# Kernel tuning notes

Hardware: AMD Instinct MI355X
Metric: run time of the kernel (lower is better)

Reference implementation:

```python
import jax, jax.numpy as jnp
import numpy as np
import math

WINDOW = 1024
B, H, E, D = 4, 8, 64, 64


def setup_inputs() -> dict:
    key = jax.random.key(0)
    kq, kk, kv, ks = jax.random.split(key, 4)
    queries = jax.random.normal(kq, (B, WINDOW, H, E), dtype=jnp.float32)
    keys = jax.random.normal(kk, (B, WINDOW, H, E), dtype=jnp.float32)
    values = jax.random.normal(kv, (B, WINDOW, H, D), dtype=jnp.float32)
    sigma = jax.random.normal(ks, (B, WINDOW, H), dtype=jnp.float32)
    return {"queries": queries, "keys": keys, "values": values, "sigma": sigma}


def reference(queries, keys, values, sigma):
    # queries: [B,L,H,E], keys: [B,S,H,E], values: [B,S,H,D], sigma: [B,L,H]
    Bq, L, Hh, Ee = queries.shape
    scale = 1.0 / math.sqrt(Ee)
    # scores: [B,H,L,S]
    attn = scale * jnp.einsum('blhe,bshe->bhls', queries, keys)
    win = attn.shape[-1]

    # sigma path: [B,L,H] -> [B,H,L]
    sig = jnp.transpose(sigma, (0, 2, 1))
    sig = jax.nn.sigmoid(sig * 5.0) + 1e-5
    sig = jnp.power(3.0, sig) - 1.0          # [B,H,L]
    sig = jnp.broadcast_to(sig[..., None], sig.shape + (win,))  # [B,H,L,S]

    # |i-j| distance matrix [L,S]
    idx = jnp.arange(win, dtype=jnp.float32)
    dist = jnp.abs(idx[:, None] - idx[None, :])

    inv_sqrt_2pi = 1.0 / math.sqrt(2.0 * math.pi)
    prior = inv_sqrt_2pi / sig * jnp.exp(-(dist ** 2) / 2.0 / (sig ** 2))

    series = jax.nn.softmax(attn, axis=-1)   # [B,H,L,S]
    V = jnp.einsum('bhls,bshd->blhd', series, values)
    return V, series, prior, sig
```

## Files before the change

kernel.cpp:

```cpp
#include <hip/hip_runtime.h>
#include <math.h>


typedef __attribute__((ext_vector_type(8))) short short8;
typedef __attribute__((ext_vector_type(4))) float f32x4;

constexpr int Bc = 4, Lc = 1024, Hc = 8, Ec = 64, Dc = 64, Sc = 1024;

constexpr long OFF_V      = 0;
constexpr long OFF_SERIES = (long)Bc * Lc * Hc * Dc;
constexpr long OFF_PRIOR  = OFF_SERIES + (long)Bc * Hc * Lc * Sc;
constexpr long OFF_SIG    = OFF_PRIOR  + (long)Bc * Hc * Lc * Sc;

constexpr long KELEMS = (long)Bc * Lc * Hc * Ec;

#define LOG2E        1.4426950408889634f
#define LOG2_3       1.5849625007211562f
#define INV_SQRT_2PI 0.3989422804014327f
#define HALF_LOG2E   0.7213475204444817f
#define FIVE_LOG2E   7.213475204444817f

#define PPITCH 258

__device__ __forceinline__ unsigned short f2bf(float x) {
    unsigned int u = __float_as_uint(x);
    return (unsigned short)((u + 0x7fffu + ((u >> 16) & 1u)) >> 16);
}
__device__ __forceinline__ float bf2f(unsigned short h) {
    return __uint_as_float(((unsigned int)h) << 16);
}
__device__ __forceinline__ void split8(const float* v, short8& hi, short8& lo) {
    #pragma unroll
    for (int j = 0; j < 8; ++j) {
        unsigned short hh = f2bf(v[j]);
        hi[j] = (short)hh;
        lo[j] = (short)f2bf(v[j] - bf2f(hh));
    }
}

__global__ __launch_bounds__(256)
void k_prep(const float* __restrict__ kp, unsigned short* __restrict__ khi,
            unsigned short* __restrict__ klo)
{
    const int i = blockIdx.x * 256 + threadIdx.x;
    const int e4 = i & 15, h = (i >> 4) & 7, s = (i >> 7) & 1023, b = i >> 17;
    const float4 v = reinterpret_cast<const float4*>(kp)[((b * Lc + s) * Hc + h) * 16 + e4];
    const unsigned short h0 = f2bf(v.x), h1 = f2bf(v.y), h2 = f2bf(v.z), h3 = f2bf(v.w);
    uint2 hi, lo;
    hi.x = (unsigned)h0 | ((unsigned)h1 << 16);
    hi.y = (unsigned)h2 | ((unsigned)h3 << 16);
    lo.x = (unsigned)f2bf(v.x - bf2f(h0)) | ((unsigned)f2bf(v.y - bf2f(h1)) << 16);
    lo.y = (unsigned)f2bf(v.z - bf2f(h2)) | ((unsigned)f2bf(v.w - bf2f(h3)) << 16);
    const long dst = ((long)(b * Hc + h) * Lc + s) * 16 + e4;
    reinterpret_cast<uint2*>(khi)[dst] = hi;
    reinterpret_cast<uint2*>(klo)[dst] = lo;
}

__global__ __launch_bounds__(256)
void v_prep(const float* __restrict__ vp, unsigned short* __restrict__ vthi,
            unsigned short* __restrict__ vtlo)
{
    __shared__ float lds[64][68];
    const int blk = blockIdx.x;
    const int bh = blk >> 4, s0 = (blk & 15) * 64;
    const int b = bh >> 3, h = bh & 7;
    const int t = threadIdx.x;
    {
        const int sl = t >> 4, d4 = t & 15;
        #pragma unroll
        for (int r = 0; r < 4; ++r) {
            const int s = sl + r * 16;
            const float4 v = reinterpret_cast<const float4*>(
                vp)[((long)(b * Lc + s0 + s) * Hc + h) * 16 + d4];
            *reinterpret_cast<float4*>(&lds[s][d4 * 4]) = v;
        }
    }
    __syncthreads();
    const int d = t >> 2, a = t & 3;
    #pragma unroll
    for (int jj = 0; jj < 4; ++jj) {
        const int sb = a * 16 + jj * 4;
        const float x0 = lds[sb + 0][d], x1 = lds[sb + 1][d];
        const float x2 = lds[sb + 2][d], x3 = lds[sb + 3][d];
        const unsigned short h0 = f2bf(x0), h1 = f2bf(x1), h2 = f2bf(x2), h3 = f2bf(x3);
        uint2 hi, lo;
        hi.x = (unsigned)h0 | ((unsigned)h1 << 16);
        hi.y = (unsigned)h2 | ((unsigned)h3 << 16);
        lo.x = (unsigned)f2bf(x0 - bf2f(h0)) | ((unsigned)f2bf(x1 - bf2f(h1)) << 16);
        lo.y = (unsigned)f2bf(x2 - bf2f(h2)) | ((unsigned)f2bf(x3 - bf2f(h3)) << 16);
        const long dst = (((long)bh * Dc + d) * Sc + s0 + sb) >> 2;
        reinterpret_cast<uint2*>(vthi)[dst] = hi;
        reinterpret_cast<uint2*>(vtlo)[dst] = lo;
    }
}

__global__ __launch_bounds__(256)
void attn_all(const float* __restrict__ qp,
              const unsigned short* __restrict__ khi,
              const unsigned short* __restrict__ klo,
              const unsigned short* __restrict__ vthi,
              const unsigned short* __restrict__ vtlo,
              const float* __restrict__ sigp, float* __restrict__ out)
{
    __shared__ float Pw_all[4][16 * PPITCH];
    __shared__ float red[4][16];

    const int bid = blockIdx.x;
    const int swz = (bid & 7) * 256 + (bid >> 3);
    const int rowblk = swz & 63, bh = swz >> 6;
    const int b = bh >> 3, h = bh & 7;
    const int row0 = rowblk * 16;
    const int t = threadIdx.x;
    const int w = t >> 6;
    const int lane = t & 63;
    const int ln = lane & 15, kg = lane >> 4;
    float* const Pw = Pw_all[w];

    short8 qhi[2], qlo[2];
    {
        const float* qrow = qp + ((long)(b * Lc + row0 + ln) * Hc + h) * Ec;
        #pragma unroll
        for (int kc = 0; kc < 2; ++kc) {
            const float* qq = qrow + kc * 32 + kg * 8;
            const float4 qa = *reinterpret_cast<const float4*>(qq);
            const float4 qb = *reinterpret_cast<const float4*>(qq + 4);
            float qv[8] = {qa.x, qa.y, qa.z, qa.w, qb.x, qb.y, qb.z, qb.w};
            split8(qv, qhi[kc], qlo[kc]);
        }
    }

    const float C = 0.125f * LOG2E;
    float sl4[4] = {0.f, 0.f, 0.f, 0.f};
    const long kcb = (long)bh * Lc;
    #pragma unroll
    for (int tt = 0; tt < 16; ++tt) {
        const int col = w * 256 + tt * 16 + ln;
        const unsigned short* kb = khi + (kcb + col) * Ec + kg * 8;
        const unsigned short* kl = klo + (kcb + col) * Ec + kg * 8;
        const short8 bh0 = *reinterpret_cast<const short8*>(kb);
        const short8 bl0 = *reinterpret_cast<const short8*>(kl);
        const short8 bh1 = *reinterpret_cast<const short8*>(kb + 32);
        const short8 bl1 = *reinterpret_cast<const short8*>(kl + 32);
        f32x4 a = {0.f, 0.f, 0.f, 0.f};
        a = __builtin_amdgcn_mfma_f32_16x16x32_bf16(qhi[0], bh0, a, 0, 0, 0);
        a = __builtin_amdgcn_mfma_f32_16x16x32_bf16(qlo[0], bh0, a, 0, 0, 0);
        a = __builtin_amdgcn_mfma_f32_16x16x32_bf16(qhi[0], bl0, a, 0, 0, 0);
        a = __builtin_amdgcn_mfma_f32_16x16x32_bf16(qhi[1], bh1, a, 0, 0, 0);
        a = __builtin_amdgcn_mfma_f32_16x16x32_bf16(qlo[1], bh1, a, 0, 0, 0);
        a = __builtin_amdgcn_mfma_f32_16x16x32_bf16(qhi[1], bl1, a, 0, 0, 0);
        #pragma unroll
        for (int i = 0; i < 4; ++i) {
            const float e = __builtin_exp2f(a[i] * C);
            sl4[i] += e;
            Pw[(kg * 4 + i) * PPITCH + tt * 16 + ln] = e;
        }
    }

    #pragma unroll
    for (int off = 1; off < 16; off <<= 1) {
        #pragma unroll
        for (int i = 0; i < 4; ++i) sl4[i] += __shfl_xor(sl4[i], off, 64);
    }
    if (ln == 0) {
        #pragma unroll
        for (int i = 0; i < 4; ++i) red[w][kg * 4 + i] = sl4[i];
    }
    __syncthreads();
    float inv4[4];
    #pragma unroll
    for (int i = 0; i < 4; ++i) {
        const int rr = kg * 4 + i;
        inv4[i] = 1.0f / (red[0][rr] + red[1][rr] + red[2][rr] + red[3][rr]);
    }

    {
        const long sbase = OFF_SERIES + ((long)bh * Lc + row0) * Sc + w * 256;
        #pragma unroll
        for (int r = 0; r < 16; ++r) {
            const float ivr = 1.0f / (red[0][r] + red[1][r] + red[2][r] + red[3][r]);
            float4 v = *reinterpret_cast<const float4*>(&Pw[r * PPITCH + lane * 4]);
            v.x *= ivr; v.y *= ivr; v.z *= ivr; v.w *= ivr;
            *reinterpret_cast<float4*>(&out[sbase + (long)r * Sc + lane * 4]) = v;
        }
    }

    short8 pahi[8], palo[8];
    #pragma unroll
    for (int kc = 0; kc < 8; ++kc) {
        const float* pa = &Pw[ln * PPITCH + kc * 32 + kg * 8];
        const float4 a0 = *reinterpret_cast<const float4*>(pa);
        const float4 a1 = *reinterpret_cast<const float4*>(pa + 4);
        float av[8] = {a0.x, a0.y, a0.z, a0.w, a1.x, a1.y, a1.z, a1.w};
        split8(av, pahi[kc], palo[kc]);
    }

    #pragma unroll
    for (int dt = 0; dt < 4; ++dt) {
        f32x4 acc = {0.f, 0.f, 0.f, 0.f};
        const long vrow = ((long)bh * Dc + dt * 16 + ln) * Sc + w * 256 + kg * 8;
        #pragma unroll
        for (int kc = 0; kc < 8; ++kc) {
            const short8 vh = *reinterpret_cast<const short8*>(vthi + vrow + kc * 32);
            const short8 vl = *reinterpret_cast<const short8*>(vtlo + vrow + kc * 32);
            acc = __builtin_amdgcn_mfma_f32_16x16x32_bf16(pahi[kc], vh, acc, 0, 0, 0);
            acc = __builtin_amdgcn_mfma_f32_16x16x32_bf16(palo[kc], vh, acc, 0, 0, 0);
            acc = __builtin_amdgcn_mfma_f32_16x16x32_bf16(pahi[kc], vl, acc, 0, 0, 0);
        }
        #pragma unroll
        for (int i = 0; i < 4; ++i)
            Pw[(kg * 4 + i) * 68 + dt * 16 + ln] = acc[i] * inv4[i];
    }
    __syncthreads();

    {
        const int r = t >> 4, d0 = (t & 15) * 4;
        const float4 s0 = *reinterpret_cast<const float4*>(&Pw_all[0][r * 68 + d0]);
        const float4 s1 = *reinterpret_cast<const float4*>(&Pw_all[1][r * 68 + d0]);
        const float4 s2 = *reinterpret_cast<const float4*>(&Pw_all[2][r * 68 + d0]);
        const float4 s3 = *reinterpret_cast<const float4*>(&Pw_all[3][r * 68 + d0]);
        float4 vs;
        vs.x = s0.x + s1.x + s2.x + s3.x;
        vs.y = s0.y + s1.y + s2.y + s3.y;
        vs.z = s0.z + s1.z + s2.z + s3.z;
        vs.w = s0.w + s1.w + s2.w + s3.w;
        *reinterpret_cast<float4*>(
            &out[OFF_V + ((long)(b * Lc + row0 + r) * Hc + h) * Dc + d0]) = vs;
    }

    {
        const int c0 = t * 4;
        #pragma unroll 4
        for (int r = 0; r < 16; ++r) {
            const int lg = row0 + r;
            const float x = sigp[(long)(b * Lc + lg) * Hc + h];
            const float sgm = 1.0f / (1.0f + __builtin_exp2f(-FIVE_LOG2E * x)) + 1e-5f;
            const float sg = __builtin_exp2f(LOG2_3 * sgm) - 1.0f;
            const float amp = INV_SQRT_2PI / sg;
            const float ce = -HALF_LOG2E / (sg * sg);
            const long rowbase = ((long)bh * Lc + lg) * Sc;
            const float df = (float)(c0 - lg);
            float4 pr;
            pr.x = amp * __builtin_exp2f(ce * df * df);
            const float d1 = df + 1.f; pr.y = amp * __builtin_exp2f(ce * d1 * d1);
            const float d2 = df + 2.f; pr.z = amp * __builtin_exp2f(ce * d2 * d2);
            const float d3 = df + 3.f; pr.w = amp * __builtin_exp2f(ce * d3 * d3);
            *reinterpret_cast<float4*>(&out[OFF_PRIOR + rowbase + c0]) = pr;
            *reinterpret_cast<float4*>(&out[OFF_SIG + rowbase + c0]) =
                make_float4(sg, sg, sg, sg);
        }
    }
}

extern "C" void kernel_launch(void* const* d_in, const int* in_sizes, int n_in,
                              void* d_out, int out_size, void* d_ws, size_t ws_size,
                              hipStream_t stream) {
    const float* q  = (const float*)d_in[0];
    const float* k  = (const float*)d_in[1];
    const float* v  = (const float*)d_in[2];
    const float* sg = (const float*)d_in[3];
    float* out = (float*)d_out;

    unsigned short* khi  = (unsigned short*)d_ws;
    unsigned short* klo  = khi + KELEMS;
    unsigned short* vthi = klo + KELEMS;
    unsigned short* vtlo = vthi + KELEMS;

    hipLaunchKernelGGL(k_prep, dim3(2048), dim3(256), 0, stream, k, khi, klo);
    hipLaunchKernelGGL(v_prep, dim3(512), dim3(256), 0, stream, v, vthi, vtlo);
    hipLaunchKernelGGL(attn_all, dim3(2048), dim3(256), 0, stream,
                       q, khi, klo, vthi, vtlo, sg, out);
}
```

Measured before the change: 553.1 us.

## Store softmax probabilities as fp16 in LDS and restructure PV loop

```diff
diff --git a/kernel.cpp b/kernel.cpp
--- a/kernel.cpp
+++ b/kernel.cpp
@@ -20,7 +20,7 @@
 #define HALF_LOG2E   0.7213475204444817f
 #define FIVE_LOG2E   7.213475204444817f
 
-#define PPITCH 258
+#define PPH 264
 
 __device__ __forceinline__ unsigned short f2bf(float x) {
     unsigned int u = __float_as_uint(x);
@@ -94,7 +94,7 @@
     }
 }
 
-__global__ __launch_bounds__(256)
+__global__ __launch_bounds__(256, 4)
 void attn_all(const float* __restrict__ qp,
               const unsigned short* __restrict__ khi,
               const unsigned short* __restrict__ klo,
@@ -102,7 +102,7 @@
               const unsigned short* __restrict__ vtlo,
               const float* __restrict__ sigp, float* __restrict__ out)
 {
-    __shared__ float Pw_all[4][16 * PPITCH];
+    __shared__ __align__(16) _Float16 P_all[4][16 * PPH];
     __shared__ float red[4][16];
 
     const int bid = blockIdx.x;
@@ -114,7 +114,7 @@
     const int w = t >> 6;
     const int lane = t & 63;
     const int ln = lane & 15, kg = lane >> 4;
-    float* const Pw = Pw_all[w];
+    _Float16* const Pw = P_all[w];
 
     short8 qhi[2], qlo[2];
     {
@@ -152,7 +152,7 @@
         for (int i = 0; i < 4; ++i) {
             const float e = __builtin_exp2f(a[i] * C);
             sl4[i] += e;
-            Pw[(kg * 4 + i) * PPITCH + tt * 16 + ln] = e;
+            Pw[(kg * 4 + i) * PPH + tt * 16 + ln] = (_Float16)e;
         }
     }
 
@@ -175,49 +175,70 @@
 
     {
         const long sbase = OFF_SERIES + ((long)bh * Lc + row0) * Sc + w * 256;
-        #pragma unroll
-        for (int r = 0; r < 16; ++r) {
+        const int colbase = lane * 8;
+        const int rofs = colbase >> 8;
+        const int col = colbase & 255;
+        #pragma unroll
+        for (int rp = 0; rp < 8; ++rp) {
+            const int r = rp * 2 + rofs;
             const float ivr = 1.0f / (red[0][r] + red[1][r] + red[2][r] + red[3][r]);
-            float4 v = *reinterpret_cast<const float4*>(&Pw[r * PPITCH + lane * 4]);
-            v.x *= ivr; v.y *= ivr; v.z *= ivr; v.w *= ivr;
-            *reinterpret_cast<float4*>(&out[sbase + (long)r * Sc + lane * 4]) = v;
-        }
-    }
-
-    short8 pahi[8], palo[8];
+            union { short8 s; _Float16 hh[8]; } u;
+            u.s = *reinterpret_cast<const short8*>(&Pw[r * PPH + col]);
+            float4 o0, o1;
+            o0.x = (float)u.hh[0] * ivr; o0.y = (float)u.hh[1] * ivr;
+            o0.z = (float)u.hh[2] * ivr; o0.w = (float)u.hh[3] * ivr;
+            o1.x = (float)u.hh[4] * ivr; o1.y = (float)u.hh[5] * ivr;
+            o1.z = (float)u.hh[6] * ivr; o1.w = (float)u.hh[7] * ivr;
+            float* dst = &out[sbase + (long)r * Sc + col];
+            *reinterpret_cast<float4*>(dst) = o0;
+            *reinterpret_cast<float4*>(dst + 4) = o1;
+        }
+    }
+
+    f32x4 acc[4];
+    #pragma unroll
+    for (int dt = 0; dt < 4; ++dt) acc[dt] = (f32x4){0.f, 0.f, 0.f, 0.f};
+    const long vbase = (long)bh * Dc * Sc + w * 256 + kg * 8;
     #pragma unroll
     for (int kc = 0; kc < 8; ++kc) {
-        const float* pa = &Pw[ln * PPITCH + kc * 32 + kg * 8];
-        const float4 a0 = *reinterpret_cast<const float4*>(pa);
-        const float4 a1 = *reinterpret_cast<const float4*>(pa + 4);
-        float av[8] = {a0.x, a0.y, a0.z, a0.w, a1.x, a1.y, a1.z, a1.w};
-        split8(av, pahi[kc], palo[kc]);
-    }
-
-    #pragma unroll
-    for (int dt = 0; dt < 4; ++dt) {
-        f32x4 acc = {0.f, 0.f, 0.f, 0.f};
-        const long vrow = ((long)bh * Dc + dt * 16 + ln) * Sc + w * 256 + kg * 8;
-        #pragma unroll
-        for (int kc = 0; kc < 8; ++kc) {
-            const short8 vh = *reinterpret_cast<const short8*>(vthi + vrow + kc * 32);
-            const short8 vl = *reinterpret_cast<const short8*>(vtlo + vrow + kc * 32);
-            acc = __builtin_amdgcn_mfma_f32_16x16x32_bf16(pahi[kc], vh, acc, 0, 0, 0);
-            acc = __builtin_amdgcn_mfma_f32_16x16x32_bf16(palo[kc], vh, acc, 0, 0, 0);
-            acc = __builtin_amdgcn_mfma_f32_16x16x32_bf16(pahi[kc], vl, acc, 0, 0, 0);
-        }
-        #pragma unroll
-        for (int i = 0; i < 4; ++i)
-            Pw[(kg * 4 + i) * 68 + dt * 16 + ln] = acc[i] * inv4[i];
+        union { short8 s; _Float16 hh[8]; } u;
+        u.s = *reinterpret_cast<const short8*>(&Pw[ln * PPH + kc * 32 + kg * 8]);
+        float av[8];
+        #pragma unroll
+        for (int j = 0; j < 8; ++j) av[j] = (float)u.hh[j];
+        short8 pahi, palo;
+        split8(av, pahi, palo);
+        #pragma unroll
+        for (int dt = 0; dt < 4; ++dt) {
+            const long vrow = vbase + (long)(dt * 16 + ln) * Sc + kc * 32;
+            const short8 vh = *reinterpret_cast<const short8*>(vthi + vrow);
+            const short8 vl = *reinterpret_cast<const short8*>(vtlo + vrow);
+            acc[dt] = __builtin_amdgcn_mfma_f32_16x16x32_bf16(pahi, vh, acc[dt], 0, 0, 0);
+            acc[dt] = __builtin_amdgcn_mfma_f32_16x16x32_bf16(palo, vh, acc[dt], 0, 0, 0);
+            acc[dt] = __builtin_amdgcn_mfma_f32_16x16x32_bf16(pahi, vl, acc[dt], 0, 0, 0);
+        }
+    }
+    {
+        float* const Pwf = reinterpret_cast<float*>(Pw);
+        #pragma unroll
+        for (int dt = 0; dt < 4; ++dt) {
+            #pragma unroll
+            for (int i = 0; i < 4; ++i)
+                Pwf[(kg * 4 + i) * 68 + dt * 16 + ln] = acc[dt][i] * inv4[i];
+        }
     }
     __syncthreads();
 
     {
         const int r = t >> 4, d0 = (t & 15) * 4;
-        const float4 s0 = *reinterpret_cast<const float4*>(&Pw_all[0][r * 68 + d0]);
-        const float4 s1 = *reinterpret_cast<const float4*>(&Pw_all[1][r * 68 + d0]);
-        const float4 s2 = *reinterpret_cast<const float4*>(&Pw_all[2][r * 68 + d0]);
-        const float4 s3 = *reinterpret_cast<const float4*>(&Pw_all[3][r * 68 + d0]);
+        const float* p0 = reinterpret_cast<const float*>(P_all[0]);
+        const float* p1 = reinterpret_cast<const float*>(P_all[1]);
+        const float* p2 = reinterpret_cast<const float*>(P_all[2]);
+        const float* p3 = reinterpret_cast<const float*>(P_all[3]);
+        const float4 s0 = *reinterpret_cast<const float4*>(&p0[r * 68 + d0]);
+        const float4 s1 = *reinterpret_cast<const float4*>(&p1[r * 68 + d0]);
+        const float4 s2 = *reinterpret_cast<const float4*>(&p2[r * 68 + d0]);
+        const float4 s3 = *reinterpret_cast<const float4*>(&p3[r * 68 + d0]);
         float4 vs;
         vs.x = s0.x + s1.x + s2.x + s3.x;
         vs.y = s0.y + s1.y + s2.y + s3.y;
```

Result: no change. 553.7 us (+0.1%).
